# Kernel tuning notes

Measured on AMD Instinct MI355X. Metric: run time of the kernel, lower is better.

Reference implementation:

```python
import jax, jax.numpy as jnp
import numpy as np

SIGMA = 30.0
N, E = 50000, 1600000
IN_LOCAL, IN_GLOBAL, HIDDEN = 128, 128, 64


def setup_inputs() -> dict:
    key = jax.random.key(0)
    ks = jax.random.split(key, 20)
    inp = {}
    inp["x_local"] = jax.random.normal(ks[0], (N, IN_LOCAL), jnp.float32)
    inp["x_global"] = jax.random.normal(ks[1], (N, IN_GLOBAL), jnp.float32)
    inp["noise_features"] = jax.random.normal(ks[2], (N, 10), jnp.float32)
    inp["coord"] = jax.random.normal(ks[3], (N, 2), jnp.float32) * 30.0
    inp["edge_index"] = jax.random.randint(ks[4], (2, E), 0, N, jnp.int32)
    # EdgeWeightLayer params (torch init: eye fc1 weight, fixed fc2 weight, zero fc2 bias)
    inp["fc1_w"] = jnp.eye(10, dtype=jnp.float32)
    inp["fc1_b"] = jax.random.uniform(ks[5], (10,), jnp.float32, -0.3, 0.3)
    inp["fc2_w"] = jnp.array([[1.0, 0.7, 0.5, 0.3, -0.5, -0.8, -0.3, -0.5, 0.2, -0.2]], jnp.float32)
    inp["fc2_b"] = jnp.zeros((1,), jnp.float32)
    sl = 1.0 / np.sqrt(IN_LOCAL)
    inp["gat_w"] = jax.random.uniform(ks[6], (HIDDEN, IN_LOCAL), jnp.float32, -sl, sl)
    inp["gat_att_src"] = jax.random.uniform(ks[7], (HIDDEN,), jnp.float32, -sl, sl)
    inp["gat_att_dst"] = jax.random.uniform(ks[8], (HIDDEN,), jnp.float32, -sl, sl)
    inp["gat_b"] = jnp.zeros((HIDDEN,), jnp.float32)
    sg = 1.0 / np.sqrt(IN_GLOBAL)
    inp["gcn_w"] = jax.random.uniform(ks[9], (HIDDEN, IN_GLOBAL), jnp.float32, -sg, sg)
    inp["gcn_b"] = jnp.zeros((HIDDEN,), jnp.float32)
    sf = 1.0 / np.sqrt(2 * HIDDEN)
    inp["fus_w1"] = jax.random.uniform(ks[10], (HIDDEN, 2 * HIDDEN), jnp.float32, -sf, sf)
    inp["fus_b1"] = jax.random.uniform(ks[11], (HIDDEN,), jnp.float32, -sf, sf)
    sh = 1.0 / np.sqrt(HIDDEN)
    inp["fus_w2"] = jax.random.uniform(ks[12], (1, HIDDEN), jnp.float32, -sh, sh)
    inp["fus_b2"] = jax.random.uniform(ks[13], (1,), jnp.float32, -sh, sh)
    return inp


def _forward(edge_index, x_local, x_global, noise_features, coord,
             fc1_w, fc1_b, fc2_w, fc2_b,
             gat_w, gat_att_src, gat_att_dst, gat_b,
             gcn_w, gcn_b, fus_w1, fus_b1, fus_w2, fus_b2):
    n = x_local.shape[0]
    src, dst = edge_index[0], edge_index[1]

    # per-edge noise MLP on gathered source node features: [E,10]->[E]
    h = jax.nn.elu(noise_features[src] @ fc1_w.T + fc1_b)
    noise_ind = (h @ fc2_w.T + fc2_b)[:, 0]

    # gaussian distance kernel + smooth mapping into [0.1, 2.0]
    d2 = jnp.sum((coord[src] - coord[dst]) ** 2, axis=1)
    gw = jnp.exp(-d2 / (2.0 * SIGMA ** 2))
    w = 0.1 + 1.9 * jax.nn.sigmoid(gw * (1.0 + noise_ind) - 1.0)
    mask = w >= 0.2  # dynamic edge masking, expressed as weight masking (jit-safe)

    # append self loops (both GATConv and GCNConv add them by default)
    loop = jnp.arange(n, dtype=src.dtype)
    s_all = jnp.concatenate([src, loop])
    d_all = jnp.concatenate([dst, loop])
    m_all = jnp.concatenate([mask, jnp.ones((n,), bool)])

    # ---- GAT branch (1 head; PyG GATConv ignores scalar edge weight when edge_dim=None) ----
    xl = x_local @ gat_w.T                           # [N, H]
    a_src = xl @ gat_att_src                         # [N]
    a_dst = xl @ gat_att_dst
    e = jax.nn.leaky_relu(a_src[s_all] + a_dst[d_all], negative_slope=0.2)
    neg = jnp.finfo(e.dtype).min
    mx = jax.ops.segment_max(jnp.where(m_all, e, neg), d_all, num_segments=n)
    ex = jnp.where(m_all, jnp.exp(e - mx[d_all]), 0.0)
    den = jax.ops.segment_sum(ex, d_all, num_segments=n)
    alpha = ex / den[d_all]
    gat_out = jax.ops.segment_sum(alpha[:, None] * xl[s_all], d_all, num_segments=n) + gat_b
    x_l = jax.nn.elu(gat_out)

    # ---- GCN branch (symmetric norm with masked edge weights, self-loop weight 1) ----
    ew = jnp.concatenate([jnp.where(mask, w, 0.0), jnp.ones((n,), w.dtype)])
    deg = jax.ops.segment_sum(ew, d_all, num_segments=n)
    dis = jnp.where(deg > 0, jax.lax.rsqrt(deg), 0.0)
    norm = dis[s_all] * ew * dis[d_all]
    xg = x_global @ gcn_w.T                          # [N, H]
    gcn_out = jax.ops.segment_sum(norm[:, None] * xg[s_all], d_all, num_segments=n) + gcn_b
    x_g = jax.nn.relu(gcn_out)

    # ---- fusion head (dropout inactive at inference) ----
    cat = jnp.concatenate([x_l, x_g], axis=1)        # [N, 2H]
    hid = jax.nn.relu(cat @ fus_w1.T + fus_b1)
    out = hid @ fus_w2.T + fus_b2                    # [N, 1]
    return out[:, 0]


def reference(x_local, x_global, noise_features, coord, edge_index,
              fc1_w, fc1_b, fc2_w, fc2_b,
              gat_w, gat_att_src, gat_att_dst, gat_b,
              gcn_w, gcn_b, fus_w1, fus_b1, fus_w2, fus_b2):
    return _forward(edge_index, x_local, x_global, noise_features, coord,
                    fc1_w, fc1_b, fc2_w, fc2_b,
                    gat_w, gat_att_src, gat_att_dst, gat_b,
                    gcn_w, gcn_b, fus_w1, fus_b1, fus_w2, fus_b2)
```

## Files before the change

kernel.cpp:

```cpp
#include <hip/hip_runtime.h>
#include <hip/hip_fp16.h>
#include <math.h>

#define NN 50000
#define NE 1600000
#define NBIN 512
#define DSTF 98
#define NREP 8
#define PCAP 24
#define BCAPR 576

__device__ __forceinline__ float wave_sum(float v) {
    #pragma unroll
    for (int off = 32; off > 0; off >>= 1) v += __shfl_xor(v, off, 64);
    return v;
}

__global__ __launch_bounds__(256) void k_node_gat(
    const float* __restrict__ x_local, const float* __restrict__ gat_w,
    const float* __restrict__ att_src, const float* __restrict__ att_dst,
    const float* __restrict__ nf, const float* __restrict__ coord,
    const float* __restrict__ fc1_w, const float* __restrict__ fc1_b,
    const float* __restrict__ fc2_w, const float* __restrict__ fc2_b,
    __half* __restrict__ xlh,
    float4* __restrict__ snode, float4* __restrict__ dnode,
    float* __restrict__ ps)
{
    __shared__ float wL[64 * 132];
    __shared__ float xt[32 * 128];
    for (int f = threadIdx.x; f < 64 * 128; f += 256) {
        int h = f >> 7, k = f & 127;
        wL[h * 132 + k] = gat_w[f];
    }
    const int lane = threadIdx.x & 63;
    const int wid  = threadIdx.x >> 6;
    const float asv = att_src[lane];
    const float adv = att_dst[lane];
    const float4* wrow = (const float4*)(wL + lane * 132);
    float4* xts = (float4*)xt;
    const float4* xp = (const float4*)x_local;
    for (int base = blockIdx.x * 32; base < NN; base += gridDim.x * 32) {
        __syncthreads();
        #pragma unroll
        for (int k = 0; k < 4; k++) {
            int gi = base * 32 + (int)threadIdx.x + k * 256;
            if (gi < NN * 32) xts[threadIdx.x + k * 256] = xp[gi];
        }
        __syncthreads();
        float acc[8] = {0.f,0.f,0.f,0.f,0.f,0.f,0.f,0.f};
        const float4* xrow = (const float4*)(xt + wid * 8 * 128);
        #pragma unroll 1
        for (int t = 0; t < 32; t++) {
            float4 wv = wrow[t];
            #pragma unroll
            for (int j = 0; j < 8; j++) {
                float4 xv = xrow[j * 32 + t];
                acc[j] = fmaf(xv.x, wv.x, acc[j]);
                acc[j] = fmaf(xv.y, wv.y, acc[j]);
                acc[j] = fmaf(xv.z, wv.z, acc[j]);
                acc[j] = fmaf(xv.w, wv.w, acc[j]);
            }
        }
        float sv[8], dv[8];
        #pragma unroll
        for (int j = 0; j < 8; j++) {
            int n = base + wid * 8 + j;
            if (n < NN) xlh[(size_t)n * 64 + lane] = __float2half(acc[j]);
            sv[j] = wave_sum(acc[j] * asv);
            dv[j] = wave_sum(acc[j] * adv);
        }
        if (lane < 8) {
            int n = base + wid * 8 + lane;
            if (n < NN) {
                float svx = (lane==0)?sv[0]:(lane==1)?sv[1]:(lane==2)?sv[2]:(lane==3)?sv[3]
                           :(lane==4)?sv[4]:(lane==5)?sv[5]:(lane==6)?sv[6]:sv[7];
                float dvx = (lane==0)?dv[0]:(lane==1)?dv[1]:(lane==2)?dv[2]:(lane==3)?dv[3]
                           :(lane==4)?dv[4]:(lane==5)?dv[5]:(lane==6)?dv[6]:dv[7];
                float xvv[10];
                #pragma unroll
                for (int k = 0; k < 10; k++) xvv[k] = nf[n * 10 + k];
                float niv = fc2_b[0];
                #pragma unroll
                for (int j = 0; j < 10; j++) {
                    float h = fc1_b[j];
                    #pragma unroll
                    for (int k = 0; k < 10; k++) h = fmaf(xvv[k], fc1_w[j * 10 + k], h);
                    h = (h > 0.f) ? h : expm1f(h);
                    niv = fmaf(h, fc2_w[j], niv);
                }
                float cx = coord[2 * n], cy = coord[2 * n + 1];
                float es = svx + dvx;
                es = (es >= 0.f) ? es : 0.2f * es;
                snode[n] = make_float4(cx, cy, svx, niv);
                dnode[n] = make_float4(cx, cy, dvx, 0.f);
                ps[n] = __expf(es);
            }
        }
    }
}

__global__ __launch_bounds__(256) void k_node_gcn(
    const float* __restrict__ x_global, const float* __restrict__ gcn_w,
    __half* __restrict__ xgh)
{
    __shared__ float wL[64 * 132];
    __shared__ float xt[32 * 128];
    for (int f = threadIdx.x; f < 64 * 128; f += 256) {
        int h = f >> 7, k = f & 127;
        wL[h * 132 + k] = gcn_w[f];
    }
    const int lane = threadIdx.x & 63;
    const int wid  = threadIdx.x >> 6;
    const float4* wrow = (const float4*)(wL + lane * 132);
    float4* xts = (float4*)xt;
    const float4* xp = (const float4*)x_global;
    for (int base = blockIdx.x * 32; base < NN; base += gridDim.x * 32) {
        __syncthreads();
        #pragma unroll
        for (int k = 0; k < 4; k++) {
            int gi = base * 32 + (int)threadIdx.x + k * 256;
            if (gi < NN * 32) xts[threadIdx.x + k * 256] = xp[gi];
        }
        __syncthreads();
        float acc[8] = {0.f,0.f,0.f,0.f,0.f,0.f,0.f,0.f};
        const float4* xrow = (const float4*)(xt + wid * 8 * 128);
        #pragma unroll 1
        for (int t = 0; t < 32; t++) {
            float4 wv = wrow[t];
            #pragma unroll
            for (int j = 0; j < 8; j++) {
                float4 xv = xrow[j * 32 + t];
                acc[j] = fmaf(xv.x, wv.x, acc[j]);
                acc[j] = fmaf(xv.y, wv.y, acc[j]);
                acc[j] = fmaf(xv.z, wv.z, acc[j]);
                acc[j] = fmaf(xv.w, wv.w, acc[j]);
            }
        }
        #pragma unroll
        for (int j = 0; j < 8; j++) {
            int n = base + wid * 8 + j;
            if (n < NN) xgh[(size_t)n * 64 + lane] = __float2half(acc[j]);
        }
    }
}

__global__ __launch_bounds__(256) void k_zerog(unsigned int* __restrict__ gcnt)
{
    int i = blockIdx.x * 256 + threadIdx.x;
    if (i < NREP * NBIN) gcnt[i] = 0u;
}

__global__ __launch_bounds__(256) void k_part2(
    const int* __restrict__ ei,
    unsigned int* __restrict__ bucket, unsigned int* __restrict__ gcnt)
{
    __shared__ unsigned int lcnt[NBIN];
    __shared__ unsigned int lbase[NBIN];
    __shared__ unsigned int lbuf[NBIN][PCAP];
    const int rep = blockIdx.x & 7;
    for (int t = threadIdx.x; t < NBIN; t += 256) lcnt[t] = 0u;
    __syncthreads();
    const int base = blockIdx.x * 2048;
    #pragma unroll
    for (int k = 0; k < 8; k++) {
        int i = base + k * 256 + threadIdx.x;
        if (i < NE) {
            int d = ei[NE + i];
            int s = ei[i];
            int b = d / DSTF;
            unsigned int pk = (unsigned int)s | ((unsigned int)(d - b * DSTF) << 16);
            unsigned int slot = atomicAdd(&lcnt[b], 1u);
            if (slot < PCAP) {
                lbuf[b][slot] = pk;
            } else {
                unsigned int g = atomicAdd(&gcnt[rep * NBIN + b], 1u);
                if (g < BCAPR) bucket[(size_t)(rep * NBIN + b) * BCAPR + g] = pk;
            }
        }
    }
    __syncthreads();
    for (int t = threadIdx.x; t < NBIN; t += 256) {
        unsigned int n = lcnt[t];
        if (n > PCAP) n = PCAP;
        lcnt[t] = n;
        lbase[t] = n ? atomicAdd(&gcnt[rep * NBIN + t], n) : 0u;
    }
    __syncthreads();
    for (int t = threadIdx.x; t < NBIN; t += 256) {
        unsigned int n = lcnt[t];
        unsigned int gb = lbase[t];
        unsigned int* dst = bucket + (size_t)(rep * NBIN + t) * BCAPR;
        for (unsigned int e = 0; e < n; e++) {
            unsigned int g = gb + e;
            if (g < BCAPR) dst[g] = lbuf[t][e];
        }
    }
}

__global__ __launch_bounds__(512) void k_edge3(
    const unsigned int* __restrict__ bucket, const unsigned int* __restrict__ gcnt,
    const float4* __restrict__ snode, const float4* __restrict__ dnode,
    uint2* __restrict__ rec, unsigned int* __restrict__ offA,
    unsigned int* __restrict__ cntA, float* __restrict__ dis)
{
    const int bin = blockIdx.x;
    const int d0  = bin * DSTF;
    __shared__ unsigned int cnt[DSTF], off[DSTF], cur[DSTF], ews[DSTF];
    __shared__ float4 dnd[DSTF];
    __shared__ unsigned int segc[NREP];
    __shared__ unsigned int sm[128];
    __shared__ unsigned int wsum[8];
    __shared__ unsigned int sbase;
    for (int t = threadIdx.x; t < DSTF; t += 512) {
        cnt[t] = 0u; cur[t] = 0u; ews[t] = 0u;
        int d = d0 + t;
        dnd[t] = (d < NN) ? dnode[d] : make_float4(0.f, 0.f, 0.f, 0.f);
    }
    if (threadIdx.x < NREP) {
        unsigned int c = gcnt[threadIdx.x * NBIN + bin];
        segc[threadIdx.x] = (c > BCAPR) ? BCAPR : c;
    }
    unsigned int partial = 0u;
    for (int idx = threadIdx.x; idx < NREP * NBIN; idx += 512) {
        int b = idx & (NBIN - 1);
        if (b < bin) {
            unsigned int c = gcnt[(idx >> 9) * NBIN + b];
            partial += (c > BCAPR) ? BCAPR : c;
        }
    }
    #pragma unroll
    for (int o = 32; o > 0; o >>= 1) partial += __shfl_xor(partial, o, 64);
    if ((threadIdx.x & 63) == 0) wsum[threadIdx.x >> 6] = partial;
    __syncthreads();
    if (threadIdx.x == 0) {
        unsigned int a = 0;
        #pragma unroll
        for (int r = 0; r < 8; r++) a += wsum[r];
        sbase = a;
    }
    __syncthreads();
    #pragma unroll
    for (int r = 0; r < NREP; r++) {
        unsigned int c = segc[r];
        const unsigned int* bk = bucket + (size_t)(r * NBIN + bin) * BCAPR;
        for (unsigned int t = threadIdx.x; t < c; t += 512)
            atomicAdd(&cnt[bk[t] >> 16], 1u);
    }
    __syncthreads();
    if (threadIdx.x < 128) sm[threadIdx.x] = (threadIdx.x < DSTF) ? cnt[threadIdx.x] : 0u;
    __syncthreads();
    for (int o = 1; o < 128; o <<= 1) {
        unsigned int t = 0;
        if (threadIdx.x < 128 && threadIdx.x >= o) t = sm[threadIdx.x - o];
        __syncthreads();
        if (threadIdx.x < 128) sm[threadIdx.x] += t;
        __syncthreads();
    }
    if (threadIdx.x < DSTF) off[threadIdx.x] = sbase + sm[threadIdx.x] - cnt[threadIdx.x];
    __syncthreads();
    #pragma unroll
    for (int r = 0; r < NREP; r++) {
        unsigned int c = segc[r];
        const unsigned int* bk = bucket + (size_t)(r * NBIN + bin) * BCAPR;
        for (unsigned int t = threadIdx.x; t < c; t += 512) {
            unsigned int pk = bk[t];
            int dl = (int)(pk >> 16);
            int s  = (int)(pk & 0xFFFFu);
            float4 sv = snode[s];
            float4 dv = dnd[dl];
            float dx = sv.x - dv.x, dy = sv.y - dv.y;
            float gw = __expf((dx * dx + dy * dy) * (-1.0f / 1800.0f));
            float tt = fmaf(gw, 1.0f + sv.w, -1.0f);
            float sg = 1.0f / (1.0f + __expf(-tt));
            float w  = fmaf(1.9f, sg, 0.1f);
            float e  = sv.z + dv.z;
            e = (e >= 0.f) ? e : 0.2f * e;
            float ewv = (w >= 0.2f) ? w : 0.0f;
            float p = (ewv != 0.f) ? __expf(e) : 0.0f;
            unsigned int rk = atomicAdd(&cur[dl], 1u);
            atomicAdd(&ews[dl], (unsigned int)(ewv * 16777216.0f + 0.5f));
            __half2 h = __floats2half2_rn(p, ewv);
            rec[off[dl] + rk] = make_uint2((unsigned int)s, *(unsigned int*)&h);
        }
    }
    __syncthreads();
    for (int t = threadIdx.x; t < DSTF; t += 512) {
        int d = d0 + t;
        if (d < NN) {
            offA[d] = off[t];
            cntA[d] = cnt[t];
            dis[d]  = rsqrtf(1.0f + (float)ews[t] * (1.0f / 16777216.0f));
        }
    }
}

__global__ __launch_bounds__(256) void k_gather2(
    const __half* __restrict__ xlh, const __half* __restrict__ xgh,
    const float* __restrict__ ps, const float* __restrict__ dis,
    const unsigned int* __restrict__ offA, const unsigned int* __restrict__ cntA,
    const uint2* __restrict__ rec,
    const float* __restrict__ gat_b, const float* __restrict__ gcn_b,
    uint2* __restrict__ catLh, uint2* __restrict__ catGh)
{
    const int lane = threadIdx.x & 63;
    const int wid  = threadIdx.x >> 6;
    const int eg   = lane >> 4;
    const int fi   = (lane & 15) << 2;
    const float4 gb = *(const float4*)(gat_b + fi);
    const float4 cb = *(const float4*)(gcn_b + fi);
    const float g0 = (eg == 0) ? 1.0f : 0.0f;
    for (int n = blockIdx.x * 4 + wid; n < NN; n += gridDim.x * 4) {
        float psv = ps[n] * g0;
        float dd = dis[n];
        int beg = (int)offA[n];
        int end = beg + (int)cntA[n];
        uint2 us = *(const uint2*)(xlh + (size_t)n * 64 + fi);
        uint2 ug = *(const uint2*)(xgh + (size_t)n * 64 + fi);
        float2 s01 = __half22float2(*(const __half2*)&us.x);
        float2 s23 = __half22float2(*(const __half2*)&us.y);
        float2 q01 = __half22float2(*(const __half2*)&ug.x);
        float2 q23 = __half22float2(*(const __half2*)&ug.y);
        float4 aL, aC;
        aL.x = psv * s01.x; aL.y = psv * s01.y; aL.z = psv * s23.x; aL.w = psv * s23.y;
        float sw = dd * g0;
        aC.x = sw * q01.x; aC.y = sw * q01.y; aC.z = sw * q23.x; aC.w = sw * q23.y;
        float den = psv;
        int j = beg + eg;
        for (; j + 4 < end; j += 8) {
            uint2 r0 = rec[j];
            uint2 r1 = rec[j + 4];
            int s0 = (int)r0.x;
            int s1 = (int)r1.x;
            float2 pc0 = __half22float2(*(const __half2*)&r0.y);
            float2 pc1 = __half22float2(*(const __half2*)&r1.y);
            float c0 = dis[s0] * pc0.y;
            float c1 = dis[s1] * pc1.y;
            uint2 ul0 = *(const uint2*)(xlh + (size_t)s0 * 64 + fi);
            uint2 ul1 = *(const uint2*)(xlh + (size_t)s1 * 64 + fi);
            uint2 ug0 = *(const uint2*)(xgh + (size_t)s0 * 64 + fi);
            uint2 ug1 = *(const uint2*)(xgh + (size_t)s1 * 64 + fi);
            float2 l0a = __half22float2(*(const __half2*)&ul0.x);
            float2 l0b = __half22float2(*(const __half2*)&ul0.y);
            float2 l1a = __half22float2(*(const __half2*)&ul1.x);
            float2 l1b = __half22float2(*(const __half2*)&ul1.y);
            float2 g0a = __half22float2(*(const __half2*)&ug0.x);
            float2 g0b = __half22float2(*(const __half2*)&ug0.y);
            float2 g1a = __half22float2(*(const __half2*)&ug1.x);
            float2 g1b = __half22float2(*(const __half2*)&ug1.y);
            aL.x = fmaf(pc0.x, l0a.x, aL.x); aL.y = fmaf(pc0.x, l0a.y, aL.y);
            aL.z = fmaf(pc0.x, l0b.x, aL.z); aL.w = fmaf(pc0.x, l0b.y, aL.w);
            aL.x = fmaf(pc1.x, l1a.x, aL.x); aL.y = fmaf(pc1.x, l1a.y, aL.y);
            aL.z = fmaf(pc1.x, l1b.x, aL.z); aL.w = fmaf(pc1.x, l1b.y, aL.w);
            aC.x = fmaf(c0, g0a.x, aC.x); aC.y = fmaf(c0, g0a.y, aC.y);
            aC.z = fmaf(c0, g0b.x, aC.z); aC.w = fmaf(c0, g0b.y, aC.w);
            aC.x = fmaf(c1, g1a.x, aC.x); aC.y = fmaf(c1, g1a.y, aC.y);
            aC.z = fmaf(c1, g1b.x, aC.z); aC.w = fmaf(c1, g1b.y, aC.w);
            den += pc0.x + pc1.x;
        }
        if (j < end) {
            uint2 r0 = rec[j];
            int s0 = (int)r0.x;
            float2 pc0 = __half22float2(*(const __half2*)&r0.y);
            float c0 = dis[s0] * pc0.y;
            uint2 ul0 = *(const uint2*)(xlh + (size_t)s0 * 64 + fi);
            uint2 ug0 = *(const uint2*)(xgh + (size_t)s0 * 64 + fi);
            float2 l0a = __half22float2(*(const __half2*)&ul0.x);
            float2 l0b = __half22float2(*(const __half2*)&ul0.y);
            float2 g0a = __half22float2(*(const __half2*)&ug0.x);
            float2 g0b = __half22float2(*(const __half2*)&ug0.y);
            aL.x = fmaf(pc0.x, l0a.x, aL.x); aL.y = fmaf(pc0.x, l0a.y, aL.y);
            aL.z = fmaf(pc0.x, l0b.x, aL.z); aL.w = fmaf(pc0.x, l0b.y, aL.w);
            aC.x = fmaf(c0, g0a.x, aC.x); aC.y = fmaf(c0, g0a.y, aC.y);
            aC.z = fmaf(c0, g0b.x, aC.z); aC.w = fmaf(c0, g0b.y, aC.w);
            den += pc0.x;
        }
        #pragma unroll
        for (int m = 16; m <= 32; m <<= 1) {
            aL.x += __shfl_xor(aL.x, m, 64); aL.y += __shfl_xor(aL.y, m, 64);
            aL.z += __shfl_xor(aL.z, m, 64); aL.w += __shfl_xor(aL.w, m, 64);
            aC.x += __shfl_xor(aC.x, m, 64); aC.y += __shfl_xor(aC.y, m, 64);
            aC.z += __shfl_xor(aC.z, m, 64); aC.w += __shfl_xor(aC.w, m, 64);
            den  += __shfl_xor(den,  m, 64);
        }
        if (eg == 0) {
            float rd = 1.0f / den;
            float4 la, ga;
            la.x = fmaf(aL.x, rd, gb.x); la.y = fmaf(aL.y, rd, gb.y);
            la.z = fmaf(aL.z, rd, gb.z); la.w = fmaf(aL.w, rd, gb.w);
            la.x = (la.x > 0.f) ? la.x : expm1f(la.x);
            la.y = (la.y > 0.f) ? la.y : expm1f(la.y);
            la.z = (la.z > 0.f) ? la.z : expm1f(la.z);
            la.w = (la.w > 0.f) ? la.w : expm1f(la.w);
            ga.x = fmaxf(fmaf(dd, aC.x, cb.x), 0.f);
            ga.y = fmaxf(fmaf(dd, aC.y, cb.y), 0.f);
            ga.z = fmaxf(fmaf(dd, aC.z, cb.z), 0.f);
            ga.w = fmaxf(fmaf(dd, aC.w, cb.w), 0.f);
            __half2 l01 = __floats2half2_rn(la.x, la.y);
            __half2 l23 = __floats2half2_rn(la.z, la.w);
            __half2 g01h = __floats2half2_rn(ga.x, ga.y);
            __half2 g23h = __floats2half2_rn(ga.z, ga.w);
            catLh[(size_t)n * 16 + (fi >> 2)] =
                make_uint2(*(unsigned int*)&l01, *(unsigned int*)&l23);
            catGh[(size_t)n * 16 + (fi >> 2)] =
                make_uint2(*(unsigned int*)&g01h, *(unsigned int*)&g23h);
        }
    }
}

__global__ __launch_bounds__(256) void k_fuse(
    const uint2* __restrict__ catLh, const uint2* __restrict__ catGh,
    const float* __restrict__ fus_w1, const float* __restrict__ fus_b1,
    const float* __restrict__ fus_w2, const float* __restrict__ fus_b2,
    float* __restrict__ out)
{
    __shared__ float wS[64 * 132];
    __shared__ uint2 catS[32 * 33];
    const int nb = blockIdx.x * 32;
    for (int f = threadIdx.x; f < 64 * 128; f += 256) {
        int r = f >> 7, c = f & 127;
        wS[r * 132 + c] = fus_w1[f];
    }
    for (int f = threadIdx.x; f < 32 * 32; f += 256) {
        int i = f >> 5, c = f & 31;
        int n = nb + i;
        uint2 v = make_uint2(0u, 0u);
        if (n < NN) v = (c < 16) ? catLh[(size_t)n * 16 + c]
                                 : catGh[(size_t)n * 16 + (c - 16)];
        catS[i * 33 + c] = v;
    }
    __syncthreads();
    const int p = threadIdx.x >> 3;
    const int q = threadIdx.x & 7;
    const int n = nb + p;
    float hid[8];
    #pragma unroll
    for (int j = 0; j < 8; j++) {
        int jj = (q + j) & 7;
        hid[j] = fus_b1[q * 8 + jj];
    }
    const uint2* cp = catS + p * 33;
    #pragma unroll 2
    for (int kb = 0; kb < 32; kb++) {
        uint2 u = cp[kb];
        float2 a = __half22float2(*(const __half2*)&u.x);
        float2 b = __half22float2(*(const __half2*)&u.y);
        #pragma unroll
        for (int j = 0; j < 8; j++) {
            int jj = (q + j) & 7;
            float4 wv = *(const float4*)(wS + (size_t)(q * 8 + jj) * 132 + kb * 4);
            hid[j] = fmaf(wv.x, a.x, hid[j]);
            hid[j] = fmaf(wv.y, a.y, hid[j]);
            hid[j] = fmaf(wv.z, b.x, hid[j]);
            hid[j] = fmaf(wv.w, b.y, hid[j]);
        }
    }
    float acc = 0.f;
    #pragma unroll
    for (int j = 0; j < 8; j++) {
        int jj = (q + j) & 7;
        acc = fmaf(fmaxf(hid[j], 0.f), fus_w2[q * 8 + jj], acc);
    }
    acc += __shfl_xor(acc, 1, 64);
    acc += __shfl_xor(acc, 2, 64);
    acc += __shfl_xor(acc, 4, 64);
    if (q == 0 && n < NN) out[n] = acc + fus_b2[0];
}

extern "C" void kernel_launch(void* const* d_in, const int* in_sizes, int n_in,
                              void* d_out, int out_size, void* d_ws, size_t ws_size,
                              hipStream_t stream)
{
    const float* x_local  = (const float*)d_in[0];
    const float* x_global = (const float*)d_in[1];
    const float* nf       = (const float*)d_in[2];
    const float* coord    = (const float*)d_in[3];
    const int*   ei       = (const int*)d_in[4];
    const float* fc1_w    = (const float*)d_in[5];
    const float* fc1_b    = (const float*)d_in[6];
    const float* fc2_w    = (const float*)d_in[7];
    const float* fc2_b    = (const float*)d_in[8];
    const float* gat_w    = (const float*)d_in[9];
    const float* att_src  = (const float*)d_in[10];
    const float* att_dst  = (const float*)d_in[11];
    const float* gat_b    = (const float*)d_in[12];
    const float* gcn_w    = (const float*)d_in[13];
    const float* gcn_b    = (const float*)d_in[14];
    const float* fus_w1   = (const float*)d_in[15];
    const float* fus_b1   = (const float*)d_in[16];
    const float* fus_w2   = (const float*)d_in[17];
    const float* fus_b2   = (const float*)d_in[18];
    float* out = (float*)d_out;

    char* ws = (char*)d_ws;
    uint2*  rec  = (uint2*) (ws);
    __half* xlh  = (__half*)(ws + 12800000);
    __half* xgh  = (__half*)(ws + 19200000);
    uint2*  catLh= (uint2*) (ws + 25600000);
    uint2*  catGh= (uint2*) (ws + 32000000);
    unsigned int* bucket = (unsigned int*)(ws + 25600000);
    float4* snode= (float4*)(ws + 38400000);
    float4* dnode= (float4*)(ws + 39200000);
    unsigned int* offA = (unsigned int*)(ws + 40000000);
    unsigned int* cntA = (unsigned int*)(ws + 40200000);
    float*  dis  = (float*) (ws + 40400000);
    float*  ps   = (float*) (ws + 40600000);
    unsigned int* gcnt = (unsigned int*)(ws + 40800000);
    (void)in_sizes; (void)n_in; (void)out_size; (void)ws_size;

    k_zerog<<<(NREP * NBIN + 255) / 256, 256, 0, stream>>>(gcnt);
    k_part2<<<782, 256, 0, stream>>>(ei, bucket, gcnt);
    k_node_gat<<<782, 256, 0, stream>>>(x_local, gat_w, att_src, att_dst,
                                        nf, coord, fc1_w, fc1_b, fc2_w, fc2_b,
                                        xlh, snode, dnode, ps);
    k_node_gcn<<<782, 256, 0, stream>>>(x_global, gcn_w, xgh);
    k_edge3<<<NBIN, 512, 0, stream>>>(bucket, gcnt, snode, dnode,
                                      rec, offA, cntA, dis);
    k_gather2<<<3125, 256, 0, stream>>>(xlh, xgh, ps, dis, offA, cntA, rec,
                                        gat_b, gcn_b, catLh, catGh);
    k_fuse<<<(NN + 31) / 32, 256, 0, stream>>>(catLh, catGh,
                                               fus_w1, fus_b1, fus_w2, fus_b2, out);
}
```

Before: 320.4 us.

## Interleave GAT and GCN node features into one row and widen gather lanes

The projected GAT and GCN half-precision features now share one 256-byte row per node (local half then global half) instead of living in two separate arrays. The gather kernel uses 8 lanes per edge with 16-byte loads, so each wave handles 8 edges at a time instead of 4. Each source-row fetch then touches one contiguous region, which should cut scattered memory transactions in the bandwidth-bound neighbour gather. The cost is more registers per lane (16 accumulators) and one extra shuffle-reduction stage.

```diff
diff --git a/kernel.cpp b/kernel.cpp
--- a/kernel.cpp
+++ b/kernel.cpp
@@ -22,7 +22,7 @@
     const float* __restrict__ nf, const float* __restrict__ coord,
     const float* __restrict__ fc1_w, const float* __restrict__ fc1_b,
     const float* __restrict__ fc2_w, const float* __restrict__ fc2_b,
-    __half* __restrict__ xlh,
+    __half* __restrict__ xch,
     float4* __restrict__ snode, float4* __restrict__ dnode,
     float* __restrict__ ps)
 {
@@ -65,7 +65,7 @@
         #pragma unroll
         for (int j = 0; j < 8; j++) {
             int n = base + wid * 8 + j;
-            if (n < NN) xlh[(size_t)n * 64 + lane] = __float2half(acc[j]);
+            if (n < NN) xch[(size_t)n * 128 + lane] = __float2half(acc[j]);
             sv[j] = wave_sum(acc[j] * asv);
             dv[j] = wave_sum(acc[j] * adv);
         }
@@ -101,7 +101,7 @@
 
 __global__ __launch_bounds__(256) void k_node_gcn(
     const float* __restrict__ x_global, const float* __restrict__ gcn_w,
-    __half* __restrict__ xgh)
+    __half* __restrict__ xch)
 {
     __shared__ float wL[64 * 132];
     __shared__ float xt[32 * 128];
@@ -139,7 +139,7 @@
         #pragma unroll
         for (int j = 0; j < 8; j++) {
             int n = base + wid * 8 + j;
-            if (n < NN) xgh[(size_t)n * 64 + lane] = __float2half(acc[j]);
+            if (n < NN) xch[(size_t)n * 128 + 64 + lane] = __float2half(acc[j]);
         }
     }
 }
@@ -294,8 +294,8 @@
     }
 }
 
-__global__ __launch_bounds__(256) void k_gather2(
-    const __half* __restrict__ xlh, const __half* __restrict__ xgh,
+__global__ __launch_bounds__(256) void k_gather3(
+    const __half* __restrict__ xch,
     const float* __restrict__ ps, const float* __restrict__ dis,
     const unsigned int* __restrict__ offA, const unsigned int* __restrict__ cntA,
     const uint2* __restrict__ rec,
@@ -304,57 +304,86 @@
 {
     const int lane = threadIdx.x & 63;
     const int wid  = threadIdx.x >> 6;
-    const int eg   = lane >> 4;
-    const int fi   = (lane & 15) << 2;
-    const float4 gb = *(const float4*)(gat_b + fi);
-    const float4 cb = *(const float4*)(gcn_b + fi);
+    const int eg   = lane >> 3;
+    const int q    = lane & 7;
+    const int fi   = q * 8;
     const float g0 = (eg == 0) ? 1.0f : 0.0f;
+    const float4 gb0 = *(const float4*)(gat_b + fi);
+    const float4 gb1 = *(const float4*)(gat_b + fi + 4);
+    const float4 cb0 = *(const float4*)(gcn_b + fi);
+    const float4 cb1 = *(const float4*)(gcn_b + fi + 4);
     for (int n = blockIdx.x * 4 + wid; n < NN; n += gridDim.x * 4) {
         float psv = ps[n] * g0;
         float dd = dis[n];
         int beg = (int)offA[n];
         int end = beg + (int)cntA[n];
-        uint2 us = *(const uint2*)(xlh + (size_t)n * 64 + fi);
-        uint2 ug = *(const uint2*)(xgh + (size_t)n * 64 + fi);
-        float2 s01 = __half22float2(*(const __half2*)&us.x);
-        float2 s23 = __half22float2(*(const __half2*)&us.y);
-        float2 q01 = __half22float2(*(const __half2*)&ug.x);
-        float2 q23 = __half22float2(*(const __half2*)&ug.y);
-        float4 aL, aC;
-        aL.x = psv * s01.x; aL.y = psv * s01.y; aL.z = psv * s23.x; aL.w = psv * s23.y;
+        const uint4* rowd = (const uint4*)(xch + (size_t)n * 128);
+        uint4 us = rowd[q];
+        uint4 ug = rowd[q + 8];
+        float2 d0 = __half22float2(*(const __half2*)&us.x);
+        float2 d1 = __half22float2(*(const __half2*)&us.y);
+        float2 d2 = __half22float2(*(const __half2*)&us.z);
+        float2 d3 = __half22float2(*(const __half2*)&us.w);
+        float2 e0 = __half22float2(*(const __half2*)&ug.x);
+        float2 e1 = __half22float2(*(const __half2*)&ug.y);
+        float2 e2 = __half22float2(*(const __half2*)&ug.z);
+        float2 e3 = __half22float2(*(const __half2*)&ug.w);
+        float aL[8], aC[8];
+        aL[0] = psv * d0.x; aL[1] = psv * d0.y; aL[2] = psv * d1.x; aL[3] = psv * d1.y;
+        aL[4] = psv * d2.x; aL[5] = psv * d2.y; aL[6] = psv * d3.x; aL[7] = psv * d3.y;
         float sw = dd * g0;
-        aC.x = sw * q01.x; aC.y = sw * q01.y; aC.z = sw * q23.x; aC.w = sw * q23.y;
+        aC[0] = sw * e0.x; aC[1] = sw * e0.y; aC[2] = sw * e1.x; aC[3] = sw * e1.y;
+        aC[4] = sw * e2.x; aC[5] = sw * e2.y; aC[6] = sw * e3.x; aC[7] = sw * e3.y;
         float den = psv;
         int j = beg + eg;
-        for (; j + 4 < end; j += 8) {
+        for (; j + 8 < end; j += 16) {
             uint2 r0 = rec[j];
-            uint2 r1 = rec[j + 4];
+            uint2 r1 = rec[j + 8];
             int s0 = (int)r0.x;
             int s1 = (int)r1.x;
             float2 pc0 = __half22float2(*(const __half2*)&r0.y);
             float2 pc1 = __half22float2(*(const __half2*)&r1.y);
             float c0 = dis[s0] * pc0.y;
             float c1 = dis[s1] * pc1.y;
-            uint2 ul0 = *(const uint2*)(xlh + (size_t)s0 * 64 + fi);
-            uint2 ul1 = *(const uint2*)(xlh + (size_t)s1 * 64 + fi);
-            uint2 ug0 = *(const uint2*)(xgh + (size_t)s0 * 64 + fi);
-            uint2 ug1 = *(const uint2*)(xgh + (size_t)s1 * 64 + fi);
-            float2 l0a = __half22float2(*(const __half2*)&ul0.x);
-            float2 l0b = __half22float2(*(const __half2*)&ul0.y);
-            float2 l1a = __half22float2(*(const __half2*)&ul1.x);
-            float2 l1b = __half22float2(*(const __half2*)&ul1.y);
-            float2 g0a = __half22float2(*(const __half2*)&ug0.x);
-            float2 g0b = __half22float2(*(const __half2*)&ug0.y);
-            float2 g1a = __half22float2(*(const __half2*)&ug1.x);
-            float2 g1b = __half22float2(*(const __half2*)&ug1.y);
-            aL.x = fmaf(pc0.x, l0a.x, aL.x); aL.y = fmaf(pc0.x, l0a.y, aL.y);
-            aL.z = fmaf(pc0.x, l0b.x, aL.z); aL.w = fmaf(pc0.x, l0b.y, aL.w);
-            aL.x = fmaf(pc1.x, l1a.x, aL.x); aL.y = fmaf(pc1.x, l1a.y, aL.y);
-            aL.z = fmaf(pc1.x, l1b.x, aL.z); aL.w = fmaf(pc1.x, l1b.y, aL.w);
-            aC.x = fmaf(c0, g0a.x, aC.x); aC.y = fmaf(c0, g0a.y, aC.y);
-            aC.z = fmaf(c0, g0b.x, aC.z); aC.w = fmaf(c0, g0b.y, aC.w);
-            aC.x = fmaf(c1, g1a.x, aC.x); aC.y = fmaf(c1, g1a.y, aC.y);
-            aC.z = fmaf(c1, g1b.x, aC.z); aC.w = fmaf(c1, g1b.y, aC.w);
+            const uint4* row0 = (const uint4*)(xch + (size_t)s0 * 128);
+            const uint4* row1 = (const uint4*)(xch + (size_t)s1 * 128);
+            uint4 l0 = row0[q];
+            uint4 g0v = row0[q + 8];
+            uint4 l1 = row1[q];
+            uint4 g1v = row1[q + 8];
+            float2 t0, t1, t2, t3;
+            t0 = __half22float2(*(const __half2*)&l0.x);
+            t1 = __half22float2(*(const __half2*)&l0.y);
+            t2 = __half22float2(*(const __half2*)&l0.z);
+            t3 = __half22float2(*(const __half2*)&l0.w);
+            aL[0] = fmaf(pc0.x, t0.x, aL[0]); aL[1] = fmaf(pc0.x, t0.y, aL[1]);
+            aL[2] = fmaf(pc0.x, t1.x, aL[2]); aL[3] = fmaf(pc0.x, t1.y, aL[3]);
+            aL[4] = fmaf(pc0.x, t2.x, aL[4]); aL[5] = fmaf(pc0.x, t2.y, aL[5]);
+            aL[6] = fmaf(pc0.x, t3.x, aL[6]); aL[7] = fmaf(pc0.x, t3.y, aL[7]);
+            t0 = __half22float2(*(const __half2*)&g0v.x);
+            t1 = __half22float2(*(const __half2*)&g0v.y);
+            t2 = __half22float2(*(const __half2*)&g0v.z);
+            t3 = __half22float2(*(const __half2*)&g0v.w);
+            aC[0] = fmaf(c0, t0.x, aC[0]); aC[1] = fmaf(c0, t0.y, aC[1]);
+            aC[2] = fmaf(c0, t1.x, aC[2]); aC[3] = fmaf(c0, t1.y, aC[3]);
+            aC[4] = fmaf(c0, t2.x, aC[4]); aC[5] = fmaf(c0, t2.y, aC[5]);
+            aC[6] = fmaf(c0, t3.x, aC[6]); aC[7] = fmaf(c0, t3.y, aC[7]);
+            t0 = __half22float2(*(const __half2*)&l1.x);
+            t1 = __half22float2(*(const __half2*)&l1.y);
+            t2 = __half22float2(*(const __half2*)&l1.z);
+            t3 = __half22float2(*(const __half2*)&l1.w);
+            aL[0] = fmaf(pc1.x, t0.x, aL[0]); aL[1] = fmaf(pc1.x, t0.y, aL[1]);
+            aL[2] = fmaf(pc1.x, t1.x, aL[2]); aL[3] = fmaf(pc1.x, t1.y, aL[3]);
+            aL[4] = fmaf(pc1.x, t2.x, aL[4]); aL[5] = fmaf(pc1.x, t2.y, aL[5]);
+            aL[6] = fmaf(pc1.x, t3.x, aL[6]); aL[7] = fmaf(pc1.x, t3.y, aL[7]);
+            t0 = __half22float2(*(const __half2*)&g1v.x);
+            t1 = __half22float2(*(const __half2*)&g1v.y);
+            t2 = __half22float2(*(const __half2*)&g1v.z);
+            t3 = __half22float2(*(const __half2*)&g1v.w);
+            aC[0] = fmaf(c1, t0.x, aC[0]); aC[1] = fmaf(c1, t0.y, aC[1]);
+            aC[2] = fmaf(c1, t1.x, aC[2]); aC[3] = fmaf(c1, t1.y, aC[3]);
+            aC[4] = fmaf(c1, t2.x, aC[4]); aC[5] = fmaf(c1, t2.y, aC[5]);
+            aC[6] = fmaf(c1, t3.x, aC[6]); aC[7] = fmaf(c1, t3.y, aC[7]);
             den += pc0.x + pc1.x;
         }
         if (j < end) {
@@ -362,47 +391,71 @@
             int s0 = (int)r0.x;
             float2 pc0 = __half22float2(*(const __half2*)&r0.y);
             float c0 = dis[s0] * pc0.y;
-            uint2 ul0 = *(const uint2*)(xlh + (size_t)s0 * 64 + fi);
-            uint2 ug0 = *(const uint2*)(xgh + (size_t)s0 * 64 + fi);
-            float2 l0a = __half22float2(*(const __half2*)&ul0.x);
-            float2 l0b = __half22float2(*(const __half2*)&ul0.y);
-            float2 g0a = __half22float2(*(const __half2*)&ug0.x);
-            float2 g0b = __half22float2(*(const __half2*)&ug0.y);
-            aL.x = fmaf(pc0.x, l0a.x, aL.x); aL.y = fmaf(pc0.x, l0a.y, aL.y);
-            aL.z = fmaf(pc0.x, l0b.x, aL.z); aL.w = fmaf(pc0.x, l0b.y, aL.w);
-            aC.x = fmaf(c0, g0a.x, aC.x); aC.y = fmaf(c0, g0a.y, aC.y);
-            aC.z = fmaf(c0, g0b.x, aC.z); aC.w = fmaf(c0, g0b.y, aC.w);
+            const uint4* row0 = (const uint4*)(xch + (size_t)s0 * 128);
+            uint4 l0 = row0[q];
+            uint4 g0v = row0[q + 8];
+            float2 t0, t1, t2, t3;
+            t0 = __half22float2(*(const __half2*)&l0.x);
+            t1 = __half22float2(*(const __half2*)&l0.y);
+            t2 = __half22float2(*(const __half2*)&l0.z);
+            t3 = __half22float2(*(const __half2*)&l0.w);
+            aL[0] = fmaf(pc0.x, t0.x, aL[0]); aL[1] = fmaf(pc0.x, t0.y, aL[1]);
+            aL[2] = fmaf(pc0.x, t1.x, aL[2]); aL[3] = fmaf(pc0.x, t1.y, aL[3]);
+            aL[4] = fmaf(pc0.x, t2.x, aL[4]); aL[5] = fmaf(pc0.x, t2.y, aL[5]);
+            aL[6] = fmaf(pc0.x, t3.x, aL[6]); aL[7] = fmaf(pc0.x, t3.y, aL[7]);
+            t0 = __half22float2(*(const __half2*)&g0v.x);
+            t1 = __half22float2(*(const __half2*)&g0v.y);
+            t2 = __half22float2(*(const __half2*)&g0v.z);
+            t3 = __half22float2(*(const __half2*)&g0v.w);
+            aC[0] = fmaf(c0, t0.x, aC[0]); aC[1] = fmaf(c0, t0.y, aC[1]);
+            aC[2] = fmaf(c0, t1.x, aC[2]); aC[3] = fmaf(c0, t1.y, aC[3]);
+            aC[4] = fmaf(c0, t2.x, aC[4]); aC[5] = fmaf(c0, t2.y, aC[5]);
+            aC[6] = fmaf(c0, t3.x, aC[6]); aC[7] = fmaf(c0, t3.y, aC[7]);
             den += pc0.x;
         }
         #pragma unroll
-        for (int m = 16; m <= 32; m <<= 1) {
-            aL.x += __shfl_xor(aL.x, m, 64); aL.y += __shfl_xor(aL.y, m, 64);
-            aL.z += __shfl_xor(aL.z, m, 64); aL.w += __shfl_xor(aL.w, m, 64);
-            aC.x += __shfl_xor(aC.x, m, 64); aC.y += __shfl_xor(aC.y, m, 64);
-            aC.z += __shfl_xor(aC.z, m, 64); aC.w += __shfl_xor(aC.w, m, 64);
-            den  += __shfl_xor(den,  m, 64);
+        for (int m = 8; m <= 32; m <<= 1) {
+            #pragma unroll
+            for (int k = 0; k < 8; k++) {
+                aL[k] += __shfl_xor(aL[k], m, 64);
+                aC[k] += __shfl_xor(aC[k], m, 64);
+            }
+            den += __shfl_xor(den, m, 64);
         }
         if (eg == 0) {
             float rd = 1.0f / den;
-            float4 la, ga;
-            la.x = fmaf(aL.x, rd, gb.x); la.y = fmaf(aL.y, rd, gb.y);
-            la.z = fmaf(aL.z, rd, gb.z); la.w = fmaf(aL.w, rd, gb.w);
-            la.x = (la.x > 0.f) ? la.x : expm1f(la.x);
-            la.y = (la.y > 0.f) ? la.y : expm1f(la.y);
-            la.z = (la.z > 0.f) ? la.z : expm1f(la.z);
-            la.w = (la.w > 0.f) ? la.w : expm1f(la.w);
-            ga.x = fmaxf(fmaf(dd, aC.x, cb.x), 0.f);
-            ga.y = fmaxf(fmaf(dd, aC.y, cb.y), 0.f);
-            ga.z = fmaxf(fmaf(dd, aC.z, cb.z), 0.f);
-            ga.w = fmaxf(fmaf(dd, aC.w, cb.w), 0.f);
-            __half2 l01 = __floats2half2_rn(la.x, la.y);
-            __half2 l23 = __floats2half2_rn(la.z, la.w);
-            __half2 g01h = __floats2half2_rn(ga.x, ga.y);
-            __half2 g23h = __floats2half2_rn(ga.z, ga.w);
-            catLh[(size_t)n * 16 + (fi >> 2)] =
+            float la[8], ga[8];
+            la[0] = fmaf(aL[0], rd, gb0.x); la[1] = fmaf(aL[1], rd, gb0.y);
+            la[2] = fmaf(aL[2], rd, gb0.z); la[3] = fmaf(aL[3], rd, gb0.w);
+            la[4] = fmaf(aL[4], rd, gb1.x); la[5] = fmaf(aL[5], rd, gb1.y);
+            la[6] = fmaf(aL[6], rd, gb1.z); la[7] = fmaf(aL[7], rd, gb1.w);
+            ga[0] = fmaxf(fmaf(dd, aC[0], cb0.x), 0.f);
+            ga[1] = fmaxf(fmaf(dd, aC[1], cb0.y), 0.f);
+            ga[2] = fmaxf(fmaf(dd, aC[2], cb0.z), 0.f);
+            ga[3] = fmaxf(fmaf(dd, aC[3], cb0.w), 0.f);
+            ga[4] = fmaxf(fmaf(dd, aC[4], cb1.x), 0.f);
+            ga[5] = fmaxf(fmaf(dd, aC[5], cb1.y), 0.f);
+            ga[6] = fmaxf(fmaf(dd, aC[6], cb1.z), 0.f);
+            ga[7] = fmaxf(fmaf(dd, aC[7], cb1.w), 0.f);
+            #pragma unroll
+            for (int k = 0; k < 8; k++)
+                la[k] = (la[k] > 0.f) ? la[k] : expm1f(la[k]);
+            __half2 l01 = __floats2half2_rn(la[0], la[1]);
+            __half2 l23 = __floats2half2_rn(la[2], la[3]);
+            __half2 l45 = __floats2half2_rn(la[4], la[5]);
+            __half2 l67 = __floats2half2_rn(la[6], la[7]);
+            __half2 g01 = __floats2half2_rn(ga[0], ga[1]);
+            __half2 g23 = __floats2half2_rn(ga[2], ga[3]);
+            __half2 g45 = __floats2half2_rn(ga[4], ga[5]);
+            __half2 g67 = __floats2half2_rn(ga[6], ga[7]);
+            catLh[(size_t)n * 16 + q * 2] =
                 make_uint2(*(unsigned int*)&l01, *(unsigned int*)&l23);
-            catGh[(size_t)n * 16 + (fi >> 2)] =
-                make_uint2(*(unsigned int*)&g01h, *(unsigned int*)&g23h);
+            catLh[(size_t)n * 16 + q * 2 + 1] =
+                make_uint2(*(unsigned int*)&l45, *(unsigned int*)&l67);
+            catGh[(size_t)n * 16 + q * 2] =
+                make_uint2(*(unsigned int*)&g01, *(unsigned int*)&g23);
+            catGh[(size_t)n * 16 + q * 2 + 1] =
+                make_uint2(*(unsigned int*)&g45, *(unsigned int*)&g67);
         }
     }
 }
@@ -493,8 +546,7 @@
 
     char* ws = (char*)d_ws;
     uint2*  rec  = (uint2*) (ws);
-    __half* xlh  = (__half*)(ws + 12800000);
-    __half* xgh  = (__half*)(ws + 19200000);
+    __half* xch  = (__half*)(ws + 12800000);
     uint2*  catLh= (uint2*) (ws + 25600000);
     uint2*  catGh= (uint2*) (ws + 32000000);
     unsigned int* bucket = (unsigned int*)(ws + 25600000);
@@ -511,11 +563,11 @@
     k_part2<<<782, 256, 0, stream>>>(ei, bucket, gcnt);
     k_node_gat<<<782, 256, 0, stream>>>(x_local, gat_w, att_src, att_dst,
                                         nf, coord, fc1_w, fc1_b, fc2_w, fc2_b,
-                                        xlh, snode, dnode, ps);
-    k_node_gcn<<<782, 256, 0, stream>>>(x_global, gcn_w, xgh);
+                                        xch, snode, dnode, ps);
+    k_node_gcn<<<782, 256, 0, stream>>>(x_global, gcn_w, xch);
     k_edge3<<<NBIN, 512, 0, stream>>>(bucket, gcnt, snode, dnode,
                                       rec, offA, cntA, dis);
-    k_gather2<<<3125, 256, 0, stream>>>(xlh, xgh, ps, dis, offA, cntA, rec,
+    k_gather3<<<3125, 256, 0, stream>>>(xch, ps, dis, offA, cntA, rec,
                                         gat_b, gcn_b, catLh, catGh);
     k_fuse<<<(NN + 31) / 32, 256, 0, stream>>>(catLh, catGh,
                                                fus_w1, fus_b1, fus_w2, fus_b2, out);
```

Measured after the change: 323.0 us. No clear change (+0.8%).
